# Kernel optimization log

Measured on AMD Instinct MI355X. Metric: run time of the kernel, lower is better.

The kernel has to match this reference:

```python
import jax, jax.numpy as jnp
import numpy as np

# Fixed generation configuration (original samples num_nodes per graph from
# dataset stats; here batched with fixed node count so shapes are static).
B, N = 64, 384                 # num_graphs, nodes per graph
NOISE, CED, HID, FEAT, NCLS = 128, 64, 512, 256, 10
DENSITY = 0.05                 # fallback density used by the original code
TEMP = 1.0                     # temperature
IU, JU = np.triu_indices(N, k=1)   # all i<j pairs, matches nested loop order
P = IU.shape[0]                # pairs per graph = N*(N-1)/2
K = int(round(DENSITY * P))    # topk edges per graph


def setup_inputs() -> dict:
    key = jax.random.key(0)
    ks = jax.random.split(key, 8)
    f32 = jnp.float32
    return {
        "z": jax.random.normal(ks[0], (B, N, NOISE), f32),
        "class_labels": jax.random.randint(ks[1], (B,), 0, NCLS),
        "embed_table": jax.random.normal(ks[2], (NCLS, CED), f32),
        "W1": jax.random.normal(ks[3], (NOISE + CED, HID), f32) / np.float32(np.sqrt(NOISE + CED)),
        "b1": jnp.zeros((HID,), f32),
        "W2": jax.random.normal(ks[4], (HID, FEAT), f32) / np.float32(np.sqrt(HID)),
        "b2": jnp.zeros((FEAT,), f32),
        "We": jax.random.normal(ks[5], (FEAT, HID), f32) / np.float32(np.sqrt(FEAT)),
        "be": jnp.zeros((HID,), f32),
        "threshold": jnp.float32(1.0),
    }


def reference(z, class_labels, embed_table, W1, b1, W2, b2, We, be, threshold):
    # class embedding, broadcast to every node of the graph
    ce = embed_table[class_labels]                               # [B, CED]
    ce = jnp.broadcast_to(ce[:, None, :], (B, N, CED))
    inp = jnp.concatenate([z, ce], axis=-1)                      # [B, N, NOISE+CED]
    # node generator: Linear -> ReLU -> Linear
    x = jax.nn.relu(inp @ W1 + b1) @ W2 + b2                     # [B, N, FEAT]
    # edge predictor encoder: Linear -> ReLU
    h = jax.nn.relu(x @ We + be)                                 # [B, N, HID]
    # pairwise L2 distances via gram trick (replaces O(n^2) torch.norm loop)
    sq = jnp.sum(h * h, axis=-1)                                 # [B, N]
    gram = jnp.einsum('bnd,bmd->bnm', h, h)                      # [B, N, N]
    d2 = jnp.maximum(sq[:, :, None] + sq[:, None, :] - 2.0 * gram, 0.0)
    dist = jnp.sqrt(jnp.maximum(d2[:, IU, JU], 1e-12))           # [B, P] upper-tri pairs
    probs = jax.nn.sigmoid((threshold - dist) / max(TEMP, 1e-6)) # [B, P]
    # per-graph top-k edge selection
    top_probs, top_idx = jax.lax.top_k(probs, K)                 # [B, K]
    iu = jnp.asarray(IU, jnp.int32)
    ju = jnp.asarray(JU, jnp.int32)
    offs = (jnp.arange(B, dtype=jnp.int32) * N)[:, None]         # node offset per graph
    u = iu[top_idx] + offs                                       # [B, K]
    v = ju[top_idx] + offs
    # per graph: [[u, v], [v, u]] (symmetrized), graphs concatenated
    row0 = jnp.concatenate([u, v], axis=1).reshape(-1)           # [B*2K]
    row1 = jnp.concatenate([v, u], axis=1).reshape(-1)
    edge_index = jnp.stack([row0, row1], axis=0)                 # [2, B*2K]
    batch = jnp.repeat(jnp.arange(B, dtype=jnp.int32), N)        # [B*N]
    return x.reshape(B * N, FEAT), edge_index, batch, top_probs
```

## Files before the change

kernel.cpp:

```cpp
#include <hip/hip_runtime.h>
#include <hip/hip_bf16.h>

#define NB    64
#define NN    384
#define PPAIR 73536
#define PRECT 147456
#define KSEL  3677
#define NSLICE 8
#define SLICEK (PRECT / NSLICE)

#define OFF_X 0
#define OFF_E 6291456
#define B2K   470656
#define OFF_B 7232768
#define OFF_P 7257344
#define TOT   7492672

#define WS_H8    0ull
#define WS_GH    0ull
#define WS_SB    4194304ull
#define WS_SQ    12582912ull
#define WS_W1P   12681216ull
#define WS_W2P   12877824ull
#define WS_WEP   13139968ull
#define WS_KEY   13402112ull
#define WS_TB    39509248ull

typedef __attribute__((ext_vector_type(8))) short bf16x8;
typedef __attribute__((ext_vector_type(4))) float f32x4;

__device__ __forceinline__ short f2bf(float f) {
    __hip_bfloat16 h = __float2bfloat16(f);
    return *reinterpret_cast<short*>(&h);
}
__device__ __forceinline__ unsigned enc8(float h) {
    if (!(h > 0.0078125f)) return 0u;
    unsigned u = __float_as_uint(h) + 0x00080000u;
    int E = (int)(u >> 23) - 127;
    if (E > 8)  return 0x7Eu;
    if (E < -6) return 0u;
    return (unsigned)(((E + 7) << 3) | ((u >> 20) & 7u));
}
__device__ __forceinline__ float dec8(unsigned b) {
    if (b == 0u) return 0.f;
    return __uint_as_float((((b >> 3) + 120u) << 23) | ((b & 7u) << 20));
}

__device__ __forceinline__ void bar_lds() {
    asm volatile("s_waitcnt lgkmcnt(0)\n\ts_barrier" ::: "memory");
}

__device__ __forceinline__ int2 pack4bf(float a, float b, float c, float d) {
    int2 pk;
    pk.x = (unsigned short)f2bf(a) | ((unsigned)(unsigned short)f2bf(b) << 16);
    pk.y = (unsigned short)f2bf(c) | ((unsigned)(unsigned short)f2bf(d) << 16);
    return pk;
}

__device__ __forceinline__ void packOne(
    const float* __restrict__ W, int K, int N, short* __restrict__ dst, int idx)
{
    if (idx >= K * N) return;
    int j = idx & 7;
    int l = (idx >> 3) & 63;
    int rest = idx >> 9;
    int Kt = K >> 5;
    int kt = rest % Kt, mt = rest / Kt;
    int k = kt * 32 + (l >> 4) * 8 + j;
    int n = mt * 16 + (l & 15);
    dst[idx] = f2bf(W[(size_t)k * N + n]);
}

__global__ __launch_bounds__(256) void pack_all_kernel(
    const float* __restrict__ W1, const float* __restrict__ W2,
    const float* __restrict__ We, short* __restrict__ W1p,
    short* __restrict__ W2p, short* __restrict__ Wep, float* __restrict__ sqW)
{
    int blk = blockIdx.x, tid = threadIdx.x;
    if (blk < 384)        packOne(W1, 192, 512, W1p, blk * 256 + tid);
    else if (blk < 896)   packOne(W2, 512, 256, W2p, (blk - 384) * 256 + tid);
    else if (blk < 1408)  packOne(We, 256, 512, Wep, (blk - 896) * 256 + tid);
    else {
        int i = (blk - 1408) * 256 + tid;
        if (i < NB * NN) sqW[i] = 0.f;
    }
}

__global__ __launch_bounds__(512, 6) void fused_mlp_kernel(
    const float* __restrict__ z, const int* __restrict__ cls,
    const float* __restrict__ et,
    const short* __restrict__ W1p, const float* __restrict__ b1,
    const short* __restrict__ W2p, const float* __restrict__ b2,
    const short* __restrict__ Wep, const float* __restrict__ be,
    float* __restrict__ xOut, unsigned char* __restrict__ h8Out,
    float* __restrict__ sqOut)
{
    __shared__ short lds[23040];
    short* A_lds  = lds;
    short* t1_lds = lds + 6400;
    short* x_lds  = lds;

    const int tid = threadIdx.x;
    const int r0 = blockIdx.x * 32;
    const int lane = tid & 63;
    const int l15 = lane & 15, kj = lane >> 4;
    const int w = tid >> 6;
    const int cl = cls[r0 / NN];

    {
        float4 v[3];
#pragma unroll
        for (int q = 0; q < 3; ++q) {
            int u = tid + q * 512;
            int row = u / 48, c4 = u - row * 48;
            int col = c4 * 4;
            const float* src = (col < 128)
                ? (z + (size_t)(r0 + row) * 128 + col)
                : (et + cl * 64 + (col - 128));
            v[q] = *(const float4*)src;
        }
#pragma unroll
        for (int q = 0; q < 3; ++q) {
            int u = tid + q * 512;
            int row = u / 48, c4 = u - row * 48;
            *(int2*)(A_lds + row * 200 + c4 * 4) =
                pack4bf(v[q].x, v[q].y, v[q].z, v[q].w);
        }
    }
    bar_lds();

    {
        f32x4 acc1[4][2];
#pragma unroll
        for (int m = 0; m < 4; ++m)
#pragma unroll
            for (int s = 0; s < 2; ++s) acc1[m][s] = (f32x4){0.f, 0.f, 0.f, 0.f};

#pragma unroll
        for (int kt = 0; kt < 6; ++kt) {
            bf16x8 bF[2];
#pragma unroll
            for (int s = 0; s < 2; ++s)
                bF[s] = *(const bf16x8*)(A_lds + (s * 16 + l15) * 200 + kt * 32 + (kj << 3));
#pragma unroll
            for (int m = 0; m < 4; ++m) {
                int mt = w * 4 + m;
                bf16x8 aF = *(const bf16x8*)(W1p + ((size_t)(mt * 6 + kt) << 9) + (lane << 3));
#pragma unroll
                for (int s = 0; s < 2; ++s)
                    acc1[m][s] = __builtin_amdgcn_mfma_f32_16x16x32_bf16(aF, bF[s], acc1[m][s], 0, 0, 0);
            }
        }
#pragma unroll
        for (int m = 0; m < 4; ++m) {
            int fl = (w * 4 + m) * 16 + (kj << 2);
            float4 bv = *(const float4*)(b1 + fl);
#pragma unroll
            for (int s = 0; s < 2; ++s) {
                int node = s * 16 + l15;
                f32x4 a = acc1[m][s];
                float v0 = fmaxf(a.x + bv.x, 0.f), v1 = fmaxf(a.y + bv.y, 0.f);
                float v2 = fmaxf(a.z + bv.z, 0.f), v3 = fmaxf(a.w + bv.w, 0.f);
                *(int2*)(t1_lds + node * 520 + fl) = pack4bf(v0, v1, v2, v3);
            }
        }
    }
    bar_lds();

    f32x4 acc2[2][2];
#pragma unroll
    for (int t = 0; t < 2; ++t)
#pragma unroll
        for (int s = 0; s < 2; ++s) acc2[t][s] = (f32x4){0.f, 0.f, 0.f, 0.f};

#pragma unroll
    for (int kt = 0; kt < 16; ++kt) {
        bf16x8 bF[2];
#pragma unroll
        for (int s = 0; s < 2; ++s)
            bF[s] = *(const bf16x8*)(t1_lds + (s * 16 + l15) * 520 + kt * 32 + (kj << 3));
#pragma unroll
        for (int t = 0; t < 2; ++t) {
            int mt = w * 2 + t;
            bf16x8 aF = *(const bf16x8*)(W2p + ((size_t)(mt * 16 + kt) << 9) + (lane << 3));
#pragma unroll
            for (int s = 0; s < 2; ++s)
                acc2[t][s] = __builtin_amdgcn_mfma_f32_16x16x32_bf16(aF, bF[s], acc2[t][s], 0, 0, 0);
        }
    }
    bar_lds();

#pragma unroll
    for (int t = 0; t < 2; ++t) {
        int feat = (w * 2 + t) * 16 + (kj << 2);
        float4 bv = *(const float4*)(b2 + feat);
#pragma unroll
        for (int s = 0; s < 2; ++s) {
            int node = s * 16 + l15;
            f32x4 a = acc2[t][s];
            float v0 = a.x + bv.x, v1 = a.y + bv.y;
            float v2 = a.z + bv.z, v3 = a.w + bv.w;
            float4 o; o.x = v0; o.y = v1; o.z = v2; o.w = v3;
            *(float4*)(xOut + (size_t)(r0 + node) * 256 + feat) = o;
            *(int2*)(x_lds + node * 264 + feat) = pack4bf(v0, v1, v2, v3);
        }
    }
    bar_lds();

    {
        f32x4 acc3[4][2];
#pragma unroll
        for (int m = 0; m < 4; ++m)
#pragma unroll
            for (int s = 0; s < 2; ++s) acc3[m][s] = (f32x4){0.f, 0.f, 0.f, 0.f};

#pragma unroll
        for (int kt = 0; kt < 8; ++kt) {
            bf16x8 bF[2];
#pragma unroll
            for (int s = 0; s < 2; ++s)
                bF[s] = *(const bf16x8*)(x_lds + (s * 16 + l15) * 264 + kt * 32 + (kj << 3));
#pragma unroll
            for (int m = 0; m < 4; ++m) {
                int mt = w * 4 + m;
                bf16x8 aF = *(const bf16x8*)(Wep + ((size_t)(mt * 8 + kt) << 9) + (lane << 3));
#pragma unroll
                for (int s = 0; s < 2; ++s)
                    acc3[m][s] = __builtin_amdgcn_mfma_f32_16x16x32_bf16(aF, bF[s], acc3[m][s], 0, 0, 0);
            }
        }
        float sqp[2] = {0.f, 0.f};
#pragma unroll
        for (int m = 0; m < 4; ++m) {
            int feat = (w * 4 + m) * 16 + (kj << 2);
            float4 bv = *(const float4*)(be + feat);
#pragma unroll
            for (int s = 0; s < 2; ++s) {
                int node = s * 16 + l15;
                f32x4 a = acc3[m][s];
                float v0 = fmaxf(a.x + bv.x, 0.f), v1 = fmaxf(a.y + bv.y, 0.f);
                float v2 = fmaxf(a.z + bv.z, 0.f), v3 = fmaxf(a.w + bv.w, 0.f);
                unsigned e0 = enc8(v0), e1 = enc8(v1), e2 = enc8(v2), e3 = enc8(v3);
                *(unsigned*)(h8Out + (size_t)(r0 + node) * 512 + feat) =
                    e0 | (e1 << 8) | (e2 << 16) | (e3 << 24);
                float h0 = dec8(e0), h1 = dec8(e1), h2 = dec8(e2), h3 = dec8(e3);
                sqp[s] += h0 * h0 + h1 * h1 + h2 * h2 + h3 * h3;
            }
        }
#pragma unroll
        for (int s = 0; s < 2; ++s) {
            float v = sqp[s];
            v += __shfl_xor(v, 16);
            v += __shfl_xor(v, 32);
            if (kj == 0)
                atomicAdd(sqOut + r0 + s * 16 + l15, v);
        }
    }
}

__global__ __launch_bounds__(512) void gram_mfma_kernel(
    const unsigned char* __restrict__ hW8, const float* __restrict__ sqW,
    unsigned short* __restrict__ keyW)
{
    extern __shared__ unsigned char smem8[];
    unsigned char* As = smem8;
    unsigned char* Bs = smem8 + 33280;

    const int tid = threadIdx.x;
    const int b  = blockIdx.x;
    int tp = blockIdx.y;
    int ti = 0; { int rem = tp; while (rem >= 6 - ti) { rem -= 6 - ti; ++ti; } tp = rem; }
    const int tj = ti + tp;
    const bool diag = (ti == tj);
    const unsigned char* Bp = diag ? As : Bs;

    const int lane = tid & 63;
    const int l15 = lane & 15, kj = lane >> 4;
    const int w = tid >> 6;
    const int mbr = (w & 3) * 16;
    const int mbc = (w >> 2) * 32;

    f32x4 acc[2];
#pragma unroll
    for (int t = 0; t < 2; ++t) acc[t] = (f32x4){0.f, 0.f, 0.f, 0.f};

    const size_t baseA = ((size_t)b * NN + ti * 64) * 512;
    const size_t baseB = ((size_t)b * NN + tj * 64) * 512;

    {
        int4 pa[4], pb[4];
#pragma unroll
        for (int q = 0; q < 4; ++q) {
            int u = tid + (q << 9);
            int row = u >> 5, g = u & 31;
            pa[q] = *(const int4*)(hW8 + baseA + row * 512 + g * 16);
            if (!diag)
                pb[q] = *(const int4*)(hW8 + baseB + row * 512 + g * 16);
        }
#pragma unroll
        for (int q = 0; q < 4; ++q) {
            int u = tid + (q << 9);
            int row = u >> 5, g = u & 31;
            *(int4*)(As + row * 520 + g * 16) = pa[q];
            if (!diag) *(int4*)(Bs + row * 520 + g * 16) = pb[q];
        }
    }
    bar_lds();

#pragma unroll
    for (int kt = 0; kt < 16; ++kt) {
        long long aF = *(const long long*)(As + (mbr + l15) * 520 + kt * 32 + kj * 8);
#pragma unroll
        for (int nt = 0; nt < 2; ++nt) {
            long long bF = *(const long long*)(Bp + (mbc + nt * 16 + l15) * 520 + kt * 32 + kj * 8);
            acc[nt] = __builtin_amdgcn_mfma_f32_16x16x32_fp8_fp8(aF, bF, acc[nt], 0, 0, 0);
        }
    }
    bar_lds();

    unsigned short* tile = (unsigned short*)smem8;
    float4 sqi = *(const float4*)(sqW + b * NN + ti * 64 + mbr + kj * 4);
    float si[4] = { sqi.x, sqi.y, sqi.z, sqi.w };
#pragma unroll
    for (int nt = 0; nt < 2; ++nt) {
        int colL = mbc + nt * 16 + l15;
        float sj = sqW[b * NN + tj * 64 + colL];
        float av[4] = { acc[nt].x, acc[nt].y, acc[nt].z, acc[nt].w };
#pragma unroll
        for (int r = 0; r < 4; ++r) {
            int rowL = mbr + kj * 4 + r;
            float d2 = fmaxf(si[r] + sj - 2.f * av[r], 0.f);
            unsigned short key = (unsigned short)(__float_as_uint(d2) >> 16);
            bool valid = !diag || (rowL < colL);
            tile[rowL * 72 + colL] = valid ? key : (unsigned short)0xFFFF;
        }
    }
    bar_lds();
    {
        int idx = tid;
        int row = idx >> 3, c8 = idx & 7;
        int4 v = *(const int4*)(tile + row * 72 + c8 * 8);
        *(int4*)(keyW + (size_t)b * PRECT + (size_t)(ti * 64 + row) * NN
                 + tj * 64 + c8 * 8) = v;
    }
}

__global__ __launch_bounds__(1024) void selA_kernel(
    const unsigned short* __restrict__ keyW, unsigned short* __restrict__ ghist)
{
    const int b = blockIdx.x, s = blockIdx.y, tid = threadIdx.x;
    const unsigned short* keys = keyW + (size_t)b * PRECT + (size_t)s * SLICEK;
    __shared__ unsigned hist[4096];
    for (int i = tid; i < 4096; i += 1024) hist[i] = 0;
    __syncthreads();
    for (int p = tid; p < SLICEK; p += 1024) {
        unsigned k = keys[p];
        if (k < 0x8000u) atomicAdd(&hist[k >> 4], 1u);
    }
    __syncthreads();
    unsigned short* dst = ghist + ((size_t)(b * NSLICE + s) << 12);
    for (int i = tid; i < 4096; i += 1024) dst[i] = (unsigned short)hist[i];
}

__global__ __launch_bounds__(1024) void selB_kernel(
    const unsigned short* __restrict__ ghist, unsigned* __restrict__ sliceBase,
    unsigned* __restrict__ Tbuf, float* __restrict__ outF)
{
    const int b = blockIdx.x, tid = threadIdx.x;
    __shared__ unsigned base[4096];
    __shared__ unsigned scanBuf[1024];
    __shared__ int sTc;
    if (tid == 0) sTc = 4095;

    unsigned c[4]; unsigned tsum = 0;
#pragma unroll
    for (int q = 0; q < 4; ++q) {
        int bin = tid * 4 + q;
        unsigned v = 0;
        for (int s = 0; s < NSLICE; ++s)
            v += ghist[((size_t)(b * NSLICE + s) << 12) + bin];
        c[q] = v; tsum += v;
    }
    scanBuf[tid] = tsum;
    __syncthreads();
    for (int o = 1; o < 1024; o <<= 1) {
        unsigned v = (tid >= o) ? scanBuf[tid - o] : 0u;
        __syncthreads();
        scanBuf[tid] += v;
        __syncthreads();
    }
    unsigned exc = scanBuf[tid] - tsum;
    {
        unsigned run = exc;
#pragma unroll
        for (int q = 0; q < 4; ++q) { base[tid * 4 + q] = run; run += c[q]; }
    }
    __syncthreads();
#pragma unroll
    for (int q = 0; q < 4; ++q) {
        int i = tid * 4 + q;
        if (base[i] < KSEL && base[i] + c[q] >= KSEL) atomicMin(&sTc, i);
    }
    __syncthreads();
    if (tid == 0) Tbuf[b] = (unsigned)sTc;

#pragma unroll
    for (int q = 0; q < 4; ++q) {
        int bin = tid * 4 + q;
        unsigned runb = base[bin];
        for (int s = 0; s < NSLICE; ++s) {
            size_t off = ((size_t)(b * NSLICE + s) << 12) + bin;
            sliceBase[off] = runb;
            runb += ghist[off];
        }
    }
    for (int i = tid; i < NN; i += 1024)
        outF[OFF_B + (size_t)b * NN + i] = (float)b;
}

__global__ __launch_bounds__(1024) void selC_emit_kernel(
    const unsigned short* __restrict__ keyW, const unsigned* __restrict__ sliceBase,
    const unsigned* __restrict__ Tbuf, const float* __restrict__ thrp,
    float* __restrict__ outF)
{
    const int b = blockIdx.x, s = blockIdx.y, tid = threadIdx.x;
    const unsigned short* keys = keyW + (size_t)b * PRECT + (size_t)s * SLICEK;
    __shared__ unsigned cnt[4096];
    const unsigned* src = sliceBase + ((size_t)(b * NSLICE + s) << 12);
    for (int i = tid; i < 4096; i += 1024) cnt[i] = src[i];
    __syncthreads();
    const int T = (int)Tbuf[b];
    const float thr0 = thrp[0];
    float* eb = outF + OFF_E + (size_t)b * (2 * KSEL);
    for (int p = tid; p < SLICEK; p += 1024) {
        unsigned k = keys[p];
        if (k < 0x8000u) {
            int bin = k >> 4;
            if (bin <= T) {
                unsigned pos = atomicAdd(&cnt[bin], 1u);
                if (pos < KSEL) {
                    int pg = s * SLICEK + p;
                    int i = pg / NN;
                    int j = pg - i * NN;
                    float u = (float)(b * NN + i);
                    float v = (float)(b * NN + j);
                    eb[pos] = u;
                    eb[KSEL + pos] = v;
                    eb[B2K + pos] = v;
                    eb[B2K + KSEL + pos] = u;
                    float d2 = __uint_as_float(((unsigned)k) << 16);
                    float dist = sqrtf(fmaxf(d2, 1e-12f));
                    outF[OFF_P + (size_t)b * KSEL + pos] =
                        1.0f / (1.0f + expf(dist - thr0));
                }
            }
        }
    }
}

extern "C" void kernel_launch(void* const* d_in, const int* in_sizes, int n_in,
                              void* d_out, int out_size, void* d_ws, size_t ws_size,
                              hipStream_t stream) {
    (void)in_sizes; (void)n_in; (void)out_size; (void)ws_size;
    const float* z   = (const float*)d_in[0];
    const int*   cls = (const int*)d_in[1];
    const float* et  = (const float*)d_in[2];
    const float* W1  = (const float*)d_in[3];
    const float* b1  = (const float*)d_in[4];
    const float* W2  = (const float*)d_in[5];
    const float* b2  = (const float*)d_in[6];
    const float* We  = (const float*)d_in[7];
    const float* be  = (const float*)d_in[8];
    const float* thr = (const float*)d_in[9];
    float* outF = (float*)d_out;

    char* w = (char*)d_ws;
    unsigned char*  hW8   = (unsigned char*)(w + WS_H8);
    float*          sqW   = (float*)(w + WS_SQ);
    short*          W1p   = (short*)(w + WS_W1P);
    short*          W2p   = (short*)(w + WS_W2P);
    short*          Wep   = (short*)(w + WS_WEP);
    unsigned short* keyW  = (unsigned short*)(w + WS_KEY);
    unsigned short* ghist = (unsigned short*)(w + WS_GH);
    unsigned*       sbase = (unsigned*)(w + WS_SB);
    unsigned*       Tbuf  = (unsigned*)(w + WS_TB);

    pack_all_kernel<<<1504, 256, 0, stream>>>(W1, W2, We, W1p, W2p, Wep, sqW);

    fused_mlp_kernel<<<768, 512, 0, stream>>>(
        z, cls, et, W1p, b1, W2p, b2, Wep, be, outF + OFF_X, hW8, sqW);

    gram_mfma_kernel<<<dim3(64, 21), 512, 66560, stream>>>(hW8, sqW, keyW);

    selA_kernel<<<dim3(64, NSLICE), 1024, 0, stream>>>(keyW, ghist);
    selB_kernel<<<64, 1024, 0, stream>>>(ghist, sbase, Tbuf, outF);
    selC_emit_kernel<<<dim3(64, NSLICE), 1024, 0, stream>>>(
        keyW, sbase, Tbuf, thr, outF);
}
```

Measured before the change: 189.4 us.

## Fuse per-slice key histogram into gram kernel epilogue, drop selA pass

Builds the per-slice 4096-bin key histogram inside the gram kernel's epilogue using LDS atomics. Each tile's counts are then flushed into a zero-initialised 32-bit global histogram with global atomics. This removes the separate selA kernel, which re-read the whole key buffer, along with one launch. In exchange it adds LDS histogram clearing, global atomic contention across tiles, and extra zeroing work in the pack kernel.

```diff
diff --git a/kernel.cpp b/kernel.cpp
--- a/kernel.cpp
+++ b/kernel.cpp
@@ -17,14 +17,14 @@
 #define TOT   7492672
 
 #define WS_H8    0ull
-#define WS_GH    0ull
 #define WS_SB    4194304ull
 #define WS_SQ    12582912ull
 #define WS_W1P   12681216ull
 #define WS_W2P   12877824ull
 #define WS_WEP   13139968ull
 #define WS_KEY   13402112ull
-#define WS_TB    39509248ull
+#define WS_GH32  32276480ull
+#define WS_TB    40665088ull
 
 typedef __attribute__((ext_vector_type(8))) short bf16x8;
 typedef __attribute__((ext_vector_type(4))) float f32x4;
@@ -74,15 +74,19 @@
 __global__ __launch_bounds__(256) void pack_all_kernel(
     const float* __restrict__ W1, const float* __restrict__ W2,
     const float* __restrict__ We, short* __restrict__ W1p,
-    short* __restrict__ W2p, short* __restrict__ Wep, float* __restrict__ sqW)
+    short* __restrict__ W2p, short* __restrict__ Wep,
+    float* __restrict__ sqW, int4* __restrict__ gh32v)
 {
     int blk = blockIdx.x, tid = threadIdx.x;
     if (blk < 384)        packOne(W1, 192, 512, W1p, blk * 256 + tid);
     else if (blk < 896)   packOne(W2, 512, 256, W2p, (blk - 384) * 256 + tid);
     else if (blk < 1408)  packOne(We, 256, 512, Wep, (blk - 896) * 256 + tid);
-    else {
+    else if (blk < 1504) {
         int i = (blk - 1408) * 256 + tid;
         if (i < NB * NN) sqW[i] = 0.f;
+    } else {
+        int i = (blk - 1504) * 256 + tid;
+        if (i < NB * NSLICE * 1024) gh32v[i] = (int4){0, 0, 0, 0};
     }
 }
 
@@ -260,7 +264,7 @@
 
 __global__ __launch_bounds__(512) void gram_mfma_kernel(
     const unsigned char* __restrict__ hW8, const float* __restrict__ sqW,
-    unsigned short* __restrict__ keyW)
+    unsigned short* __restrict__ keyW, unsigned* __restrict__ ghist32)
 {
     extern __shared__ unsigned char smem8[];
     unsigned char* As = smem8;
@@ -319,6 +323,11 @@
     bar_lds();
 
     unsigned short* tile = (unsigned short*)smem8;
+    unsigned* hs = (unsigned*)(smem8 + 33280);
+    for (int i = tid; i < 8192; i += 512) hs[i] = 0;
+    bar_lds();
+
+    const int s0 = (ti * 64) / 48;
     float4 sqi = *(const float4*)(sqW + b * NN + ti * 64 + mbr + kj * 4);
     float si[4] = { sqi.x, sqi.y, sqi.z, sqi.w };
 #pragma unroll
@@ -333,6 +342,10 @@
             unsigned short key = (unsigned short)(__float_as_uint(d2) >> 16);
             bool valid = !diag || (rowL < colL);
             tile[rowL * 72 + colL] = valid ? key : (unsigned short)0xFFFF;
+            if (valid && key < (unsigned short)0x8000u) {
+                int sl = ((ti * 64 + rowL) / 48) - s0;
+                atomicAdd(&hs[(sl << 12) + (key >> 4)], 1u);
+            }
         }
     }
     bar_lds();
@@ -343,27 +356,16 @@
         *(int4*)(keyW + (size_t)b * PRECT + (size_t)(ti * 64 + row) * NN
                  + tj * 64 + c8 * 8) = v;
     }
-}
-
-__global__ __launch_bounds__(1024) void selA_kernel(
-    const unsigned short* __restrict__ keyW, unsigned short* __restrict__ ghist)
-{
-    const int b = blockIdx.x, s = blockIdx.y, tid = threadIdx.x;
-    const unsigned short* keys = keyW + (size_t)b * PRECT + (size_t)s * SLICEK;
-    __shared__ unsigned hist[4096];
-    for (int i = tid; i < 4096; i += 1024) hist[i] = 0;
-    __syncthreads();
-    for (int p = tid; p < SLICEK; p += 1024) {
-        unsigned k = keys[p];
-        if (k < 0x8000u) atomicAdd(&hist[k >> 4], 1u);
-    }
-    __syncthreads();
-    unsigned short* dst = ghist + ((size_t)(b * NSLICE + s) << 12);
-    for (int i = tid; i < 4096; i += 1024) dst[i] = (unsigned short)hist[i];
+    for (int i = tid; i < 4096; i += 512) {
+        unsigned v0 = hs[i];
+        if (v0) atomicAdd(&ghist32[((size_t)(b * NSLICE + s0) << 12) + i], v0);
+        unsigned v1 = hs[4096 + i];
+        if (v1) atomicAdd(&ghist32[((size_t)(b * NSLICE + s0 + 1) << 12) + i], v1);
+    }
 }
 
 __global__ __launch_bounds__(1024) void selB_kernel(
-    const unsigned short* __restrict__ ghist, unsigned* __restrict__ sliceBase,
+    const unsigned* __restrict__ ghist32, unsigned* __restrict__ sliceBase,
     unsigned* __restrict__ Tbuf, float* __restrict__ outF)
 {
     const int b = blockIdx.x, tid = threadIdx.x;
@@ -378,7 +380,7 @@
         int bin = tid * 4 + q;
         unsigned v = 0;
         for (int s = 0; s < NSLICE; ++s)
-            v += ghist[((size_t)(b * NSLICE + s) << 12) + bin];
+            v += ghist32[((size_t)(b * NSLICE + s) << 12) + bin];
         c[q] = v; tsum += v;
     }
     scanBuf[tid] = tsum;
@@ -411,7 +413,7 @@
         for (int s = 0; s < NSLICE; ++s) {
             size_t off = ((size_t)(b * NSLICE + s) << 12) + bin;
             sliceBase[off] = runb;
-            runb += ghist[off];
+            runb += ghist32[off];
         }
     }
     for (int i = tid; i < NN; i += 1024)
@@ -481,19 +483,19 @@
     short*          W2p   = (short*)(w + WS_W2P);
     short*          Wep   = (short*)(w + WS_WEP);
     unsigned short* keyW  = (unsigned short*)(w + WS_KEY);
-    unsigned short* ghist = (unsigned short*)(w + WS_GH);
+    unsigned*       gh32  = (unsigned*)(w + WS_GH32);
     unsigned*       sbase = (unsigned*)(w + WS_SB);
     unsigned*       Tbuf  = (unsigned*)(w + WS_TB);
 
-    pack_all_kernel<<<1504, 256, 0, stream>>>(W1, W2, We, W1p, W2p, Wep, sqW);
+    pack_all_kernel<<<3552, 256, 0, stream>>>(
+        W1, W2, We, W1p, W2p, Wep, sqW, (int4*)gh32);
 
     fused_mlp_kernel<<<768, 512, 0, stream>>>(
         z, cls, et, W1p, b1, W2p, b2, Wep, be, outF + OFF_X, hW8, sqW);
 
-    gram_mfma_kernel<<<dim3(64, 21), 512, 66560, stream>>>(hW8, sqW, keyW);
-
-    selA_kernel<<<dim3(64, NSLICE), 1024, 0, stream>>>(keyW, ghist);
-    selB_kernel<<<64, 1024, 0, stream>>>(ghist, sbase, Tbuf, outF);
+    gram_mfma_kernel<<<dim3(64, 21), 512, 66560, stream>>>(hW8, sqW, keyW, gh32);
+
+    selB_kernel<<<64, 1024, 0, stream>>>(gh32, sbase, Tbuf, outF);
     selC_emit_kernel<<<dim3(64, NSLICE), 1024, 0, stream>>>(
         keyW, sbase, Tbuf, thr, outF);
 }
```

Result: faster. 185.2 us (-2.2%).
